# Performance work log

Measured on AMD Instinct MI355X. Metric: run time of the kernel, lower is better.

## Reference

```python
import jax, jax.numpy as jnp
import numpy as np
from jax import lax

# fixed finite-difference kernels (HWIO)
KXN = jnp.asarray([[0., -1., 1.]], dtype=jnp.float32).reshape(1, 3, 1, 1)
KXP = jnp.asarray([[-1., 1., 0.]], dtype=jnp.float32).reshape(1, 3, 1, 1)
KYN = jnp.asarray([[1.], [-1.], [0.]], dtype=jnp.float32).reshape(3, 1, 1, 1)
KYP = jnp.asarray([[0.], [1.], [-1.]], dtype=jnp.float32).reshape(3, 1, 1, 1)


def conv2d(x, k):
    # NHWC input, HWIO kernel, SAME padding, stride 1
    return lax.conv_general_dilated(x, k, (1, 1), 'SAME',
                                    dimension_numbers=('NHWC', 'HWIO', 'NHWC'))


def setup_inputs() -> dict:
    key = jax.random.key(0)
    ks = jax.random.split(key, 11)
    B, H, W = 8, 512, 512
    return {
        'u': jax.random.normal(ks[0], (B, H, W, 1), jnp.float32),
        'image': jax.random.uniform(ks[1], (B, H, W, 1), jnp.float32),
        'conv_kernel_x': jax.random.normal(ks[2], (3, 3, 1, 32), jnp.float32) * 0.05,
        'conv_kernel_y': jax.random.normal(ks[3], (3, 3, 1, 32), jnp.float32) * 0.05,
        'sep_kernel_depthwise': jax.random.normal(ks[4], (3, 3, 1, 8), jnp.float32) * 0.05,
        'sep_kernel_pointwise': jax.random.normal(ks[5], (1, 1, 8, 8), jnp.float32) * 0.05,
        'conv_kernel_curve_0': jax.random.normal(ks[6], (5, 5, 1, 8), jnp.float32) * 0.05,
        'conv_kernel_curve_1': jax.random.normal(ks[7], (5, 5, 8, 8), jnp.float32) * 0.05,
        'conv_kernel_curve_2': jax.random.normal(ks[8], (3, 3, 8, 16), jnp.float32) * 0.05,
        'conv_kernel_smoother': jax.random.normal(ks[9], (5, 5, 1, 1), jnp.float32) * 0.05,
        'kappa_kernel': jax.random.normal(ks[10], (H, W, 1), jnp.float32) * 0.05,
    }


def reference(u, image, conv_kernel_x, conv_kernel_y, sep_kernel_depthwise,
              sep_kernel_pointwise, conv_kernel_curve_0, conv_kernel_curve_1,
              conv_kernel_curve_2, conv_kernel_smoother, kappa_kernel):
    # separable conv on the (fixed) image: in_ch=1 so depthwise == standard conv
    edges = conv2d(conv2d(image, sep_kernel_depthwise), sep_kernel_pointwise)
    edges = jnp.sum(jax.nn.relu(edges), axis=-1, keepdims=True)
    edges = jax.nn.soft_sign(edges)  # x / (1 + |x|)

    grad_edges_x = jnp.sum(jax.nn.relu(conv2d(edges, conv_kernel_x)), axis=-1, keepdims=True)
    grad_edges_y = jnp.sum(jax.nn.relu(conv2d(edges, conv_kernel_y)), axis=-1, keepdims=True)

    xp = conv2d(u, KXP)
    xn = conv2d(u, KXN)
    yp = conv2d(u, KYP)
    yn = conv2d(u, KYN)

    fxp = jax.nn.relu(grad_edges_x)
    fxn = -jax.nn.relu(-grad_edges_x)
    fyp = jax.nn.relu(grad_edges_y)
    fyn = -jax.nn.relu(-grad_edges_y)

    kappa = conv2d(conv2d(conv2d(u, conv_kernel_curve_0), conv_kernel_curve_1), conv_kernel_curve_2)
    kappa = jnp.sum(kappa, axis=-1, keepdims=True)
    kappa = kappa * kappa_kernel  # (H,W,1) broadcasts over batch
    kappa = conv2d(kappa, conv_kernel_smoother)

    return u + fxp * xp + fxn * xn + fyp * yp + fyn * yn + edges + kappa
```

## Files before the change

### kernel.cpp

```cpp
#include <hip/hip_runtime.h>
#include <cstddef>

#define HH 512
#define WW 512
#define BB 8
#define T  32

#define F0    256
#define E0    1280
#define MAPW  520
#define MAPB  (512 * MAPW)
#define K0    (E0 + BB * MAPB)
#define WS_NEEDED_BYTES ((size_t)(K0 + BB * MAPB) * 4)

typedef __attribute__((ext_vector_type(8))) short short8;
typedef __attribute__((ext_vector_type(4))) float float4v;

__device__ inline unsigned short f2bf(float f) {
  unsigned u = __builtin_bit_cast(unsigned, f);
  unsigned r = (u + 0x7FFFu + ((u >> 16) & 1u)) >> 16;
  return (unsigned short)r;
}

__global__ __launch_bounds__(256) void precompute_kernels(
    const float* __restrict__ kd,
    const float* __restrict__ kp,
    const float* __restrict__ k0,
    const float* __restrict__ k1,
    const float* __restrict__ k2,
    const float* __restrict__ kx,
    const float* __restrict__ ky,
    float* __restrict__ ws) {
  __shared__ float k9[648];
  __shared__ float k2s[72];
  const int tid = threadIdx.x;

  for (int idx = tid; idx < 72; idx += 256) {
    int c = idx & 7, pq = idx >> 3;
    float s = 0.f;
    for (int c0 = 0; c0 < 8; ++c0) s = fmaf(kd[pq * 8 + c0], kp[c0 * 8 + c], s);
    ws[idx] = s;
  }
  for (int idx = tid; idx < 72; idx += 256) {
    int c1 = idx & 7, tv = idx >> 3;
    float s = 0.f;
    for (int c2 = 0; c2 < 16; ++c2) s += k2[(tv * 8 + c1) * 16 + c2];
    k2s[idx] = s;
  }
  for (int idx = tid; idx < 648; idx += 256) {
    int c1 = idx & 7;
    int ab = idx >> 3;
    int a = ab / 9, b = ab % 9;
    float s = 0.f;
    int plo = a > 4 ? a - 4 : 0, phi = a < 4 ? a : 4;
    int qlo = b > 4 ? b - 4 : 0, qhi = b < 4 ? b : 4;
    for (int p = plo; p <= phi; ++p)
      for (int q = qlo; q <= qhi; ++q) {
        int r = a - p, sx = b - q;
        const float* k0p = &k0[(p * 5 + q) * 8];
        const float* k1p = &k1[((r * 5 + sx) * 8) * 8 + c1];
        for (int c0 = 0; c0 < 8; ++c0) s = fmaf(k0p[c0], k1p[c0 * 8], s);
      }
    k9[idx] = s;
  }
  for (int idx = tid; idx < 2048; idx += 256) {
    int nt = idx >> 9, ln = (idx >> 3) & 63, j = idx & 7;
    int k = (ln >> 4) * 8 + j;
    int n = nt * 16 + (ln & 15);
    float v = 0.f;
    if (k < 9) v = (n < 32) ? kx[k * 32 + n] : ky[k * 32 + (n - 32)];
    ((unsigned short*)ws)[F0 * 2 + idx] = f2bf(v);
  }
  __syncthreads();
  for (int idx = tid; idx < 121; idx += 256) {
    int A = idx / 11, B = idx % 11;
    float s = 0.f;
    int tlo = A > 8 ? A - 8 : 0, thi = A < 2 ? A : 2;
    int vlo = B > 8 ? B - 8 : 0, vhi = B < 2 ? B : 2;
    for (int t = tlo; t <= thi; ++t)
      for (int v = vlo; v <= vhi; ++v) {
        int a = A - t, b = B - v;
        for (int c1 = 0; c1 < 8; ++c1)
          s = fmaf(k9[(a * 9 + b) * 8 + c1], k2s[(t * 3 + v) * 8 + c1], s);
      }
    ws[72 + idx] = s;
  }
}

__global__ __launch_bounds__(256) void kernelA(
    const float* __restrict__ u, const float* __restrict__ img,
    const float* __restrict__ kk, const float* ws,
    float* maps) {
  __shared__ float su[42 * 44];
  __shared__ float si[34 * 36];

  const int bx = blockIdx.x * T, by = blockIdx.y * T, b = blockIdx.z;
  const int tid = threadIdx.x;
  const float* ub = u + (size_t)b * HH * WW;
  const float* ib = img + (size_t)b * HH * WW;

  for (int idx = tid; idx < 42 * 42; idx += 256) {
    int i = idx / 42, j = idx % 42;
    int gy = by - 5 + i, gx = bx - 5 + j;
    float v = 0.f;
    if ((unsigned)gy < HH && (unsigned)gx < WW) v = ub[gy * WW + gx];
    su[i * 44 + j] = v;
  }
  for (int idx = tid; idx < 34 * 34; idx += 256) {
    int i = idx / 34, j = idx % 34;
    int gy = by - 1 + i, gx = bx - 1 + j;
    float v = 0.f;
    if ((unsigned)gy < HH && (unsigned)gx < WW) v = ib[gy * WW + gx];
    si[i * 36 + j] = v;
  }
  __syncthreads();

  const int oy = tid >> 3, ox = (tid & 7) * 4;
  const int gy = by + oy, gx = bx + ox;

  float acc[8][4];
  #pragma unroll
  for (int c = 0; c < 8; ++c)
    #pragma unroll
    for (int t = 0; t < 4; ++t) acc[c][t] = 0.f;
  #pragma unroll
  for (int p = 0; p < 3; ++p) {
    const float* srow = &si[(oy + p) * 36 + ox];
    float4 r4 = *reinterpret_cast<const float4*>(srow);
    float2 r2 = *reinterpret_cast<const float2*>(srow + 4);
    float r[6] = {r4.x, r4.y, r4.z, r4.w, r2.x, r2.y};
    #pragma unroll
    for (int q = 0; q < 3; ++q) {
      float4 w0 = *reinterpret_cast<const float4*>(&ws[(p * 3 + q) * 8]);
      float4 w1 = *reinterpret_cast<const float4*>(&ws[(p * 3 + q) * 8 + 4]);
      #pragma unroll
      for (int t = 0; t < 4; ++t) {
        float v = r[q + t];
        acc[0][t] = fmaf(v, w0.x, acc[0][t]);
        acc[1][t] = fmaf(v, w0.y, acc[1][t]);
        acc[2][t] = fmaf(v, w0.z, acc[2][t]);
        acc[3][t] = fmaf(v, w0.w, acc[3][t]);
        acc[4][t] = fmaf(v, w1.x, acc[4][t]);
        acc[5][t] = fmaf(v, w1.y, acc[5][t]);
        acc[6][t] = fmaf(v, w1.z, acc[6][t]);
        acc[7][t] = fmaf(v, w1.w, acc[7][t]);
      }
    }
  }
  float ev[4];
  #pragma unroll
  for (int t = 0; t < 4; ++t) {
    float e = 0.f;
    #pragma unroll
    for (int c = 0; c < 8; ++c) e += fmaxf(acc[c][t], 0.f);
    ev[t] = e / (1.f + e);
  }
  float* erow = maps + E0 + (size_t)b * MAPB + (size_t)gy * MAPW + 4 + gx;
  *reinterpret_cast<float4*>(erow) = make_float4(ev[0], ev[1], ev[2], ev[3]);

  float o0 = 0.f, o1 = 0.f, o2 = 0.f, o3 = 0.f;
  #pragma unroll
  for (int A = 0; A < 11; ++A) {
    const float* row = &su[(oy + A) * 44 + ox];
    float4 v0 = *reinterpret_cast<const float4*>(row);
    float4 v1 = *reinterpret_cast<const float4*>(row + 4);
    float4 v2 = *reinterpret_cast<const float4*>(row + 8);
    float2 v3 = *reinterpret_cast<const float2*>(row + 12);
    float r[14] = {v0.x, v0.y, v0.z, v0.w, v1.x, v1.y, v1.z, v1.w,
                   v2.x, v2.y, v2.z, v2.w, v3.x, v3.y};
    #pragma unroll
    for (int B2 = 0; B2 < 11; ++B2) {
      float w = ws[72 + A * 11 + B2];
      o0 = fmaf(r[B2],     w, o0);
      o1 = fmaf(r[B2 + 1], w, o1);
      o2 = fmaf(r[B2 + 2], w, o2);
      o3 = fmaf(r[B2 + 3], w, o3);
    }
  }
  float4 kkv = *reinterpret_cast<const float4*>(&kk[(size_t)gy * WW + gx]);
  float* krow = maps + K0 + (size_t)b * MAPB + (size_t)gy * MAPW + 4 + gx;
  *reinterpret_cast<float4*>(krow) =
      make_float4(o0 * kkv.x, o1 * kkv.y, o2 * kkv.z, o3 * kkv.w);

  if (bx == 0 && (tid & 7) == 0) {
    float4 z = make_float4(0.f, 0.f, 0.f, 0.f);
    *reinterpret_cast<float4*>(maps + E0 + (size_t)b * MAPB + (size_t)gy * MAPW) = z;
    *reinterpret_cast<float4*>(maps + K0 + (size_t)b * MAPB + (size_t)gy * MAPW) = z;
  }
  if (bx == WW - T && (tid & 7) == 7) {
    float4 z = make_float4(0.f, 0.f, 0.f, 0.f);
    *reinterpret_cast<float4*>(maps + E0 + (size_t)b * MAPB + (size_t)gy * MAPW + 516) = z;
    *reinterpret_cast<float4*>(maps + K0 + (size_t)b * MAPB + (size_t)gy * MAPW + 516) = z;
  }
}

__global__ __launch_bounds__(256) void kernelB(
    const float* __restrict__ u,
    const float* __restrict__ sm,
    const float* maps, float* __restrict__ out) {
  __shared__ float sgx[32 * 32];
  __shared__ float sgy[32 * 32];

  const int bx = blockIdx.x * T, by = blockIdx.y * T, b = blockIdx.z;
  const int tid = threadIdx.x;
  const float* emap = maps + E0 + (size_t)b * MAPB;
  const float* kmap = maps + K0 + (size_t)b * MAPB;
  const float* ub   = u + (size_t)b * HH * WW;

  const int lane = tid & 63;
  const int wv   = tid >> 6;
  const int q    = lane >> 4;
  const int m    = lane & 15;

  short8 afr[4];
  {
    const unsigned short* F = ((const unsigned short*)maps) + F0 * 2;
    #pragma unroll
    for (int t = 0; t < 4; ++t)
      afr[t] = *reinterpret_cast<const short8*>(F + (t * 64 + lane) * 8);
  }

  const int gy0 = by + wv * 8;

  #pragma unroll
  for (int h = 0; h < 32; h += 16) {
    const int gxl = bx + h + m;
    const float* colp = emap + 4 + gxl - 1;

    unsigned short W[9];
    #pragma unroll
    for (int d = 0; d < 3; ++d) {
      int ry = gy0 - 1 + d;
      int rc = ry < 0 ? 0 : (ry > HH - 1 ? HH - 1 : ry);
      float msk = (ry == rc) ? 1.f : 0.f;
      const float* rp = colp + (size_t)rc * MAPW;
      W[3 * d + 0] = f2bf(rp[0] * msk);
      W[3 * d + 1] = f2bf(rp[1] * msk);
      W[3 * d + 2] = f2bf(rp[2] * msk);
    }

    #pragma unroll
    for (int r = 0; r < 8; ++r) {
      short8 bv = (short8)0;
      if (q == 0) {
        #pragma unroll
        for (int j = 0; j < 8; ++j) bv[j] = (short)W[j];
      } else if (q == 1) {
        bv[0] = (short)W[8];
      }

      float4v c0 = {0.f, 0.f, 0.f, 0.f}, c1 = c0, c2 = c0, c3 = c0;
      c0 = __builtin_amdgcn_mfma_f32_16x16x32_bf16(afr[0], bv, c0, 0, 0, 0);
      c1 = __builtin_amdgcn_mfma_f32_16x16x32_bf16(afr[1], bv, c1, 0, 0, 0);
      c2 = __builtin_amdgcn_mfma_f32_16x16x32_bf16(afr[2], bv, c2, 0, 0, 0);
      c3 = __builtin_amdgcn_mfma_f32_16x16x32_bf16(afr[3], bv, c3, 0, 0, 0);

      float rx = 0.f, ry = 0.f;
      #pragma unroll
      for (int i = 0; i < 4; ++i) {
        rx += fmaxf(c0[i], 0.f) + fmaxf(c1[i], 0.f);
        ry += fmaxf(c2[i], 0.f) + fmaxf(c3[i], 0.f);
      }
      rx += __shfl_xor(rx, 16); rx += __shfl_xor(rx, 32);
      ry += __shfl_xor(ry, 16); ry += __shfl_xor(ry, 32);

      if (q == 0) {
        sgx[(wv * 8 + r) * 32 + h + m] = rx;
        sgy[(wv * 8 + r) * 32 + h + m] = ry;
      }

      if (r < 7) {
        #pragma unroll
        for (int t = 0; t < 6; ++t) W[t] = W[t + 3];
        int ryn = gy0 + r + 2;
        int rcn = ryn < 0 ? 0 : (ryn > HH - 1 ? HH - 1 : ryn);
        float msk = (ryn == rcn) ? 1.f : 0.f;
        const float* rp = colp + (size_t)rcn * MAPW;
        W[6] = f2bf(rp[0] * msk);
        W[7] = f2bf(rp[1] * msk);
        W[8] = f2bf(rp[2] * msk);
      }
    }
  }
  __syncthreads();

  {
    const int oy = tid >> 3, ox = (tid & 7) * 4;
    const int gy = by + oy, gx = bx + ox;

    float4 gx4 = *reinterpret_cast<const float4*>(&sgx[oy * 32 + ox]);
    float4 gy4 = *reinterpret_cast<const float4*>(&sgy[oy * 32 + ox]);
    float gxa[4] = {gx4.x, gx4.y, gx4.z, gx4.w};
    float gya[4] = {gy4.x, gy4.y, gy4.z, gy4.w};

    float4 ec4 = *reinterpret_cast<const float4*>(&emap[(size_t)gy * MAPW + 4 + gx]);
    float ec[4] = {ec4.x, ec4.y, ec4.z, ec4.w};

    float kap[4] = {0.f, 0.f, 0.f, 0.f};
    #pragma unroll
    for (int m5 = 0; m5 < 5; ++m5) {
      int ry = gy - 2 + m5;
      int rc = ry < 0 ? 0 : (ry > HH - 1 ? HH - 1 : ry);
      float msk = (ry == rc) ? 1.f : 0.f;
      const float* row = kmap + (size_t)rc * MAPW + 4 + gx;
      float2 a  = *reinterpret_cast<const float2*>(row - 2);
      float4 c4 = *reinterpret_cast<const float4*>(row);
      float2 d2 = *reinterpret_cast<const float2*>(row + 4);
      float r[8] = {a.x, a.y, c4.x, c4.y, c4.z, c4.w, d2.x, d2.y};
      #pragma unroll
      for (int n = 0; n < 5; ++n) {
        float w = sm[m5 * 5 + n] * msk;
        #pragma unroll
        for (int t = 0; t < 4; ++t) kap[t] = fmaf(r[t + n], w, kap[t]);
      }
    }

    const float* ur = ub + (size_t)gy * WW + gx;
    float4 uc4 = *reinterpret_cast<const float4*>(ur);
    int jm = gx > 0 ? -1 : 0;
    float ul = ur[jm];
    ul = gx > 0 ? ul : 0.f;
    int ryd = gy < HH - 1 ? gy + 1 : HH - 1;
    float md = gy < HH - 1 ? 1.f : 0.f;
    float4 ud4 = *reinterpret_cast<const float4*>(ub + (size_t)ryd * WW + gx);

    float uc[4]  = {uc4.x, uc4.y, uc4.z, uc4.w};
    float ulx[4] = {ul, uc4.x, uc4.y, uc4.z};
    float udn[4] = {ud4.x * md, ud4.y * md, ud4.z * md, ud4.w * md};

    float res[4];
    #pragma unroll
    for (int t = 0; t < 4; ++t) {
      float xp = uc[t] - ulx[t];
      float yp = uc[t] - udn[t];
      res[t] = uc[t] + gxa[t] * xp + gya[t] * yp + ec[t] + kap[t];
    }
    *reinterpret_cast<float4*>(&out[((size_t)b * HH + gy) * WW + gx]) =
        make_float4(res[0], res[1], res[2], res[3]);
  }
}

__global__ __launch_bounds__(256) void forcing_main(
    const float* __restrict__ u, const float* __restrict__ img,
    const float* __restrict__ kx, const float* __restrict__ ky,
    const float* __restrict__ sm, const float* __restrict__ kk,
    const float* __restrict__ ws, float* __restrict__ out) {
  __shared__ float su[46][48];
  __shared__ float si[36][37];
  __shared__ float se[34][35];
  __shared__ float sk[36][37];
  __shared__ float w_edge[72];
  __shared__ float w_kx[288];
  __shared__ float w_ky[288];
  __shared__ float w_k11[124];
  __shared__ float w_sm[28];

  const int bx = blockIdx.x * T;
  const int by = blockIdx.y * T;
  const int b  = blockIdx.z;
  const int tid = threadIdx.x;
  const float* ub = u   + (size_t)b * HH * WW;
  const float* ib = img + (size_t)b * HH * WW;

  for (int i = tid; i < 72; i += 256)  w_edge[i] = ws[i];
  for (int i = tid; i < 121; i += 256) w_k11[i]  = ws[72 + i];
  for (int i = tid; i < 288; i += 256) { w_kx[i] = kx[i]; w_ky[i] = ky[i]; }
  if (tid < 25) w_sm[tid] = sm[tid];

  for (int idx = tid; idx < 46 * 46; idx += 256) {
    int i = idx / 46, j = idx % 46;
    int gy = by - 7 + i, gx = bx - 7 + j;
    float v = 0.f;
    if ((unsigned)gy < HH && (unsigned)gx < WW) v = ub[gy * WW + gx];
    su[i][j] = v;
  }
  for (int idx = tid; idx < 36 * 36; idx += 256) {
    int i = idx / 36, j = idx % 36;
    int gy = by - 2 + i, gx = bx - 2 + j;
    float v = 0.f;
    if ((unsigned)gy < HH && (unsigned)gx < WW) v = ib[gy * WW + gx];
    si[i][j] = v;
  }
  __syncthreads();

  for (int idx = tid; idx < 34 * 9; idx += 256) {
    int i = idx / 9, j0 = (idx % 9) * 4;
    float acc[8][4];
    #pragma unroll
    for (int c = 0; c < 8; ++c)
      #pragma unroll
      for (int t = 0; t < 4; ++t) acc[c][t] = 0.f;
    #pragma unroll
    for (int p = 0; p < 3; ++p) {
      float r[6];
      #pragma unroll
      for (int t = 0; t < 6; ++t) r[t] = si[i + p][j0 + t];
      #pragma unroll
      for (int q = 0; q < 3; ++q) {
        const float4 w0 = *reinterpret_cast<const float4*>(&w_edge[(p * 3 + q) * 8]);
        const float4 w1 = *reinterpret_cast<const float4*>(&w_edge[(p * 3 + q) * 8 + 4]);
        #pragma unroll
        for (int t = 0; t < 4; ++t) {
          float v = r[q + t];
          acc[0][t] = fmaf(v, w0.x, acc[0][t]);
          acc[1][t] = fmaf(v, w0.y, acc[1][t]);
          acc[2][t] = fmaf(v, w0.z, acc[2][t]);
          acc[3][t] = fmaf(v, w0.w, acc[3][t]);
          acc[4][t] = fmaf(v, w1.x, acc[4][t]);
          acc[5][t] = fmaf(v, w1.y, acc[5][t]);
          acc[6][t] = fmaf(v, w1.z, acc[6][t]);
          acc[7][t] = fmaf(v, w1.w, acc[7][t]);
        }
      }
    }
    int gy = by - 1 + i;
    #pragma unroll
    for (int t = 0; t < 4; ++t) {
      int j = j0 + t;
      if (j < 34) {
        int gx = bx - 1 + j;
        float val = 0.f;
        if ((unsigned)gy < HH && (unsigned)gx < WW) {
          float e = 0.f;
          #pragma unroll
          for (int c = 0; c < 8; ++c) e += fmaxf(acc[c][t], 0.f);
          val = e / (1.f + e);
        }
        se[i][j] = val;
      }
    }
  }

  for (int idx = tid; idx < 36 * 9; idx += 256) {
    int i = idx / 9, js = (idx % 9) * 4;
    float o0 = 0.f, o1 = 0.f, o2 = 0.f, o3 = 0.f;
    #pragma unroll
    for (int A = 0; A < 11; ++A) {
      const float* row = &su[i + A][js];
      float4 v0 = *reinterpret_cast<const float4*>(row);
      float4 v1 = *reinterpret_cast<const float4*>(row + 4);
      float4 v2 = *reinterpret_cast<const float4*>(row + 8);
      float r[14] = {v0.x, v0.y, v0.z, v0.w, v1.x, v1.y, v1.z, v1.w,
                     v2.x, v2.y, v2.z, v2.w, row[12], row[13]};
      #pragma unroll
      for (int B2 = 0; B2 < 11; ++B2) {
        float w = w_k11[A * 11 + B2];
        o0 = fmaf(r[B2],     w, o0);
        o1 = fmaf(r[B2 + 1], w, o1);
        o2 = fmaf(r[B2 + 2], w, o2);
        o3 = fmaf(r[B2 + 3], w, o3);
      }
    }
    int gy = by - 2 + i;
    float o[4] = {o0, o1, o2, o3};
    #pragma unroll
    for (int t = 0; t < 4; ++t) {
      int gx = bx - 2 + js + t;
      float val = 0.f;
      if ((unsigned)gy < HH && (unsigned)gx < WW) val = o[t] * kk[gy * WW + gx];
      sk[i][js + t] = val;
    }
  }
  __syncthreads();

  {
    const int oy = tid >> 3;
    const int ox = (tid & 7) * 4;
    const int gy = by + oy;
    const int gx = bx + ox;

    float e[3][6];
    #pragma unroll
    for (int p = 0; p < 3; ++p)
      #pragma unroll
      for (int t = 0; t < 6; ++t) e[p][t] = se[oy + p][ox + t];

    const float4* wx4 = reinterpret_cast<const float4*>(w_kx);
    const float4* wy4 = reinterpret_cast<const float4*>(w_ky);

    float gxa[4] = {0.f, 0.f, 0.f, 0.f};
    float gya[4] = {0.f, 0.f, 0.f, 0.f};
    #pragma unroll
    for (int cq = 0; cq < 8; ++cq) {
      float sx[4][4], sy[4][4];
      #pragma unroll
      for (int cc = 0; cc < 4; ++cc)
        #pragma unroll
        for (int t = 0; t < 4; ++t) { sx[cc][t] = 0.f; sy[cc][t] = 0.f; }
      #pragma unroll
      for (int p = 0; p < 3; ++p)
        #pragma unroll
        for (int q = 0; q < 3; ++q) {
          float4 wx = wx4[(p * 3 + q) * 8 + cq];
          float4 wy = wy4[(p * 3 + q) * 8 + cq];
          #pragma unroll
          for (int t = 0; t < 4; ++t) {
            float evv = e[p][q + t];
            sx[0][t] = fmaf(evv, wx.x, sx[0][t]);
            sx[1][t] = fmaf(evv, wx.y, sx[1][t]);
            sx[2][t] = fmaf(evv, wx.z, sx[2][t]);
            sx[3][t] = fmaf(evv, wx.w, sx[3][t]);
            sy[0][t] = fmaf(evv, wy.x, sy[0][t]);
            sy[1][t] = fmaf(evv, wy.y, sy[1][t]);
            sy[2][t] = fmaf(evv, wy.z, sy[2][t]);
            sy[3][t] = fmaf(evv, wy.w, sy[3][t]);
          }
        }
      #pragma unroll
      for (int cc = 0; cc < 4; ++cc)
        #pragma unroll
        for (int t = 0; t < 4; ++t) {
          gxa[t] += fmaxf(sx[cc][t], 0.f);
          gya[t] += fmaxf(sy[cc][t], 0.f);
        }
    }

    float res[4];
    #pragma unroll
    for (int t = 0; t < 4; ++t) {
      float kap = 0.f;
      #pragma unroll
      for (int m = 0; m < 5; ++m)
        #pragma unroll
        for (int n = 0; n < 5; ++n)
          kap = fmaf(sk[oy + m][ox + t + n], w_sm[m * 5 + n], kap);

      float uc = su[oy + 7][ox + 7 + t];
      float xp = uc - su[oy + 7][ox + 6 + t];
      float yp = uc - su[oy + 8][ox + 7 + t];
      float ec = se[oy + 1][ox + 1 + t];
      res[t] = uc + gxa[t] * xp + gya[t] * yp + ec + kap;
    }

    float4 r4 = make_float4(res[0], res[1], res[2], res[3]);
    *reinterpret_cast<float4*>(&out[((size_t)b * HH + gy) * WW + gx]) = r4;
  }
}

extern "C" void kernel_launch(void* const* d_in, const int* in_sizes, int n_in,
                              void* d_out, int out_size, void* d_ws, size_t ws_size,
                              hipStream_t stream) {
  const float* u   = (const float*)d_in[0];
  const float* img = (const float*)d_in[1];
  const float* kx  = (const float*)d_in[2];
  const float* ky  = (const float*)d_in[3];
  const float* kd  = (const float*)d_in[4];
  const float* kp  = (const float*)d_in[5];
  const float* k0  = (const float*)d_in[6];
  const float* k1  = (const float*)d_in[7];
  const float* k2  = (const float*)d_in[8];
  const float* sm  = (const float*)d_in[9];
  const float* kk  = (const float*)d_in[10];
  float* out = (float*)d_out;
  float* ws  = (float*)d_ws;

  precompute_kernels<<<1, 256, 0, stream>>>(kd, kp, k0, k1, k2, kx, ky, ws);
  dim3 grid(WW / T, HH / T, BB);
  if (ws != nullptr && ws_size >= WS_NEEDED_BYTES) {
    kernelA<<<grid, 256, 0, stream>>>(u, img, kk, ws, ws);
    kernelB<<<grid, 256, 0, stream>>>(u, sm, ws, out);
  } else {
    forcing_main<<<grid, 256, 0, stream>>>(u, img, kx, ky, sm, kk, ws, out);
  }
}
```

Measured before the change: 154.2 us.

## Compute 11x11 kappa convolution in kernelA with bf16 MFMA instead of FP32 FMAs

Replaces the scalar 11x11 effective-kernel convolution on u with a banded Toeplitz matrix product on bf16 MFMA 16x16x32 instructions. The precompute kernel now builds a bf16 Toeplitz weight table in the workspace, and u is staged transposed in LDS as bf16. This cuts the FP32 FMA work and LDS reads per output, but lowers the precision of the kappa path to bf16 inputs and adds strided transposed LDS stores.

```diff
diff --git a/kernel.cpp b/kernel.cpp
--- a/kernel.cpp
+++ b/kernel.cpp
@@ -7,7 +7,8 @@
 #define T  32
 
 #define F0    256
-#define E0    1280
+#define KT0   1280
+#define E0    4096
 #define MAPW  520
 #define MAPB  (512 * MAPW)
 #define K0    (E0 + BB * MAPB)
@@ -33,6 +34,7 @@
     float* __restrict__ ws) {
   __shared__ float k9[648];
   __shared__ float k2s[72];
+  __shared__ float kef[121];
   const int tid = threadIdx.x;
 
   for (int idx = tid; idx < 72; idx += 256) {
@@ -84,6 +86,16 @@
           s = fmaf(k9[(a * 9 + b) * 8 + c1], k2s[(t * 3 + v) * 8 + c1], s);
       }
     ws[72 + idx] = s;
+    kef[idx] = s;
+  }
+  __syncthreads();
+  for (int idx = tid; idx < 5632; idx += 256) {
+    int b = idx >> 9, ln = (idx >> 3) & 63, j = idx & 7;
+    int m = ln & 15;
+    int k = (ln >> 4) * 8 + j;
+    int a = k - m - 3;
+    float v = ((unsigned)a < 11u) ? kef[a * 11 + b] : 0.f;
+    ((unsigned short*)ws)[KT0 * 2 + idx] = f2bf(v);
   }
 }
 
@@ -91,7 +103,7 @@
     const float* __restrict__ u, const float* __restrict__ img,
     const float* __restrict__ kk, const float* ws,
     float* maps) {
-  __shared__ float su[42 * 44];
+  __shared__ unsigned short suT[42 * 56];
   __shared__ float si[34 * 36];
 
   const int bx = blockIdx.x * T, by = blockIdx.y * T, b = blockIdx.z;
@@ -99,12 +111,12 @@
   const float* ub = u + (size_t)b * HH * WW;
   const float* ib = img + (size_t)b * HH * WW;
 
-  for (int idx = tid; idx < 42 * 42; idx += 256) {
-    int i = idx / 42, j = idx % 42;
-    int gy = by - 5 + i, gx = bx - 5 + j;
+  for (int idx = tid; idx < 48 * 42; idx += 256) {
+    int r = idx / 42, c = idx % 42;
+    int gy = by - 8 + r, gx = bx - 5 + c;
     float v = 0.f;
     if ((unsigned)gy < HH && (unsigned)gx < WW) v = ub[gy * WW + gx];
-    su[i * 44 + j] = v;
+    suT[c * 56 + r] = f2bf(v);
   }
   for (int idx = tid; idx < 34 * 34; idx += 256) {
     int i = idx / 34, j = idx % 34;
@@ -115,82 +127,86 @@
   }
   __syncthreads();
 
-  const int oy = tid >> 3, ox = (tid & 7) * 4;
-  const int gy = by + oy, gx = bx + ox;
-
-  float acc[8][4];
-  #pragma unroll
-  for (int c = 0; c < 8; ++c)
-    #pragma unroll
-    for (int t = 0; t < 4; ++t) acc[c][t] = 0.f;
-  #pragma unroll
-  for (int p = 0; p < 3; ++p) {
-    const float* srow = &si[(oy + p) * 36 + ox];
-    float4 r4 = *reinterpret_cast<const float4*>(srow);
-    float2 r2 = *reinterpret_cast<const float2*>(srow + 4);
-    float r[6] = {r4.x, r4.y, r4.z, r4.w, r2.x, r2.y};
-    #pragma unroll
-    for (int q = 0; q < 3; ++q) {
-      float4 w0 = *reinterpret_cast<const float4*>(&ws[(p * 3 + q) * 8]);
-      float4 w1 = *reinterpret_cast<const float4*>(&ws[(p * 3 + q) * 8 + 4]);
-      #pragma unroll
-      for (int t = 0; t < 4; ++t) {
-        float v = r[q + t];
-        acc[0][t] = fmaf(v, w0.x, acc[0][t]);
-        acc[1][t] = fmaf(v, w0.y, acc[1][t]);
-        acc[2][t] = fmaf(v, w0.z, acc[2][t]);
-        acc[3][t] = fmaf(v, w0.w, acc[3][t]);
-        acc[4][t] = fmaf(v, w1.x, acc[4][t]);
-        acc[5][t] = fmaf(v, w1.y, acc[5][t]);
-        acc[6][t] = fmaf(v, w1.z, acc[6][t]);
-        acc[7][t] = fmaf(v, w1.w, acc[7][t]);
-      }
-    }
-  }
-  float ev[4];
-  #pragma unroll
-  for (int t = 0; t < 4; ++t) {
-    float e = 0.f;
-    #pragma unroll
-    for (int c = 0; c < 8; ++c) e += fmaxf(acc[c][t], 0.f);
-    ev[t] = e / (1.f + e);
-  }
-  float* erow = maps + E0 + (size_t)b * MAPB + (size_t)gy * MAPW + 4 + gx;
-  *reinterpret_cast<float4*>(erow) = make_float4(ev[0], ev[1], ev[2], ev[3]);
-
-  float o0 = 0.f, o1 = 0.f, o2 = 0.f, o3 = 0.f;
-  #pragma unroll
-  for (int A = 0; A < 11; ++A) {
-    const float* row = &su[(oy + A) * 44 + ox];
-    float4 v0 = *reinterpret_cast<const float4*>(row);
-    float4 v1 = *reinterpret_cast<const float4*>(row + 4);
-    float4 v2 = *reinterpret_cast<const float4*>(row + 8);
-    float2 v3 = *reinterpret_cast<const float2*>(row + 12);
-    float r[14] = {v0.x, v0.y, v0.z, v0.w, v1.x, v1.y, v1.z, v1.w,
-                   v2.x, v2.y, v2.z, v2.w, v3.x, v3.y};
-    #pragma unroll
-    for (int B2 = 0; B2 < 11; ++B2) {
-      float w = ws[72 + A * 11 + B2];
-      o0 = fmaf(r[B2],     w, o0);
-      o1 = fmaf(r[B2 + 1], w, o1);
-      o2 = fmaf(r[B2 + 2], w, o2);
-      o3 = fmaf(r[B2 + 3], w, o3);
-    }
-  }
-  float4 kkv = *reinterpret_cast<const float4*>(&kk[(size_t)gy * WW + gx]);
-  float* krow = maps + K0 + (size_t)b * MAPB + (size_t)gy * MAPW + 4 + gx;
-  *reinterpret_cast<float4*>(krow) =
-      make_float4(o0 * kkv.x, o1 * kkv.y, o2 * kkv.z, o3 * kkv.w);
-
-  if (bx == 0 && (tid & 7) == 0) {
-    float4 z = make_float4(0.f, 0.f, 0.f, 0.f);
-    *reinterpret_cast<float4*>(maps + E0 + (size_t)b * MAPB + (size_t)gy * MAPW) = z;
-    *reinterpret_cast<float4*>(maps + K0 + (size_t)b * MAPB + (size_t)gy * MAPW) = z;
-  }
-  if (bx == WW - T && (tid & 7) == 7) {
-    float4 z = make_float4(0.f, 0.f, 0.f, 0.f);
-    *reinterpret_cast<float4*>(maps + E0 + (size_t)b * MAPB + (size_t)gy * MAPW + 516) = z;
-    *reinterpret_cast<float4*>(maps + K0 + (size_t)b * MAPB + (size_t)gy * MAPW + 516) = z;
+  {
+    const int oy = tid >> 3, ox = (tid & 7) * 4;
+    const int gy = by + oy, gx = bx + ox;
+
+    float acc[8][4];
+    #pragma unroll
+    for (int c = 0; c < 8; ++c)
+      #pragma unroll
+      for (int t = 0; t < 4; ++t) acc[c][t] = 0.f;
+    #pragma unroll
+    for (int p = 0; p < 3; ++p) {
+      const float* srow = &si[(oy + p) * 36 + ox];
+      float4 r4 = *reinterpret_cast<const float4*>(srow);
+      float2 r2 = *reinterpret_cast<const float2*>(srow + 4);
+      float r[6] = {r4.x, r4.y, r4.z, r4.w, r2.x, r2.y};
+      #pragma unroll
+      for (int q = 0; q < 3; ++q) {
+        float4 w0 = *reinterpret_cast<const float4*>(&ws[(p * 3 + q) * 8]);
+        float4 w1 = *reinterpret_cast<const float4*>(&ws[(p * 3 + q) * 8 + 4]);
+        #pragma unroll
+        for (int t = 0; t < 4; ++t) {
+          float v = r[q + t];
+          acc[0][t] = fmaf(v, w0.x, acc[0][t]);
+          acc[1][t] = fmaf(v, w0.y, acc[1][t]);
+          acc[2][t] = fmaf(v, w0.z, acc[2][t]);
+          acc[3][t] = fmaf(v, w0.w, acc[3][t]);
+          acc[4][t] = fmaf(v, w1.x, acc[4][t]);
+          acc[5][t] = fmaf(v, w1.y, acc[5][t]);
+          acc[6][t] = fmaf(v, w1.z, acc[6][t]);
+          acc[7][t] = fmaf(v, w1.w, acc[7][t]);
+        }
+      }
+    }
+    float ev[4];
+    #pragma unroll
+    for (int t = 0; t < 4; ++t) {
+      float e = 0.f;
+      #pragma unroll
+      for (int c = 0; c < 8; ++c) e += fmaxf(acc[c][t], 0.f);
+      ev[t] = e / (1.f + e);
+    }
+    float* erow = maps + E0 + (size_t)b * MAPB + (size_t)gy * MAPW + 4 + gx;
+    *reinterpret_cast<float4*>(erow) = make_float4(ev[0], ev[1], ev[2], ev[3]);
+
+    if (bx == 0 && (tid & 7) == 0) {
+      float4 z = make_float4(0.f, 0.f, 0.f, 0.f);
+      *reinterpret_cast<float4*>(maps + E0 + (size_t)b * MAPB + (size_t)gy * MAPW) = z;
+      *reinterpret_cast<float4*>(maps + K0 + (size_t)b * MAPB + (size_t)gy * MAPW) = z;
+    }
+    if (bx == WW - T && (tid & 7) == 7) {
+      float4 z = make_float4(0.f, 0.f, 0.f, 0.f);
+      *reinterpret_cast<float4*>(maps + E0 + (size_t)b * MAPB + (size_t)gy * MAPW + 516) = z;
+      *reinterpret_cast<float4*>(maps + K0 + (size_t)b * MAPB + (size_t)gy * MAPW + 516) = z;
+    }
+  }
+
+  {
+    const int lane = tid & 63;
+    const int wv   = tid >> 6;
+    const int q    = lane >> 4;
+    const int n    = lane & 15;
+    const int sty  = wv >> 1, stx = wv & 1;
+
+    const unsigned short* KT = ((const unsigned short*)ws) + KT0 * 2;
+
+    float4v acc = {0.f, 0.f, 0.f, 0.f};
+    #pragma unroll
+    for (int bb = 0; bb < 11; ++bb) {
+      short8 af = *reinterpret_cast<const short8*>(KT + (bb * 64 + lane) * 8);
+      short8 bf = *reinterpret_cast<const short8*>(
+          &suT[(stx * 16 + n + bb) * 56 + sty * 16 + q * 8]);
+      acc = __builtin_amdgcn_mfma_f32_16x16x32_bf16(af, bf, acc, 0, 0, 0);
+    }
+    float* kmapb = maps + K0 + (size_t)b * MAPB;
+    #pragma unroll
+    for (int i = 0; i < 4; ++i) {
+      int yy = by + sty * 16 + q * 4 + i;
+      int xx = bx + stx * 16 + n;
+      kmapb[(size_t)yy * MAPW + 4 + xx] = acc[i] * kk[(size_t)yy * WW + xx];
+    }
   }
 }
 
```

After: 143.8 us. -6.7%, faster.
